# Optimization experiments

Hardware: AMD Instinct MI355X
Metric: run time of the kernel (lower is better)

The kernel has to match this reference:

```python
import jax, jax.numpy as jnp
import numpy as np

D_X, N_LAYERS, N_HEADS, D_OUT = 1024, 4, 16, 1024
D_H = D_X // N_HEADS
LN_EPS = 1e-5


def _layernorm(x, g, b):
    mu = jnp.mean(x, axis=-1, keepdims=True)
    var = jnp.var(x, axis=-1, keepdims=True)
    return (x - mu) * jax.lax.rsqrt(var + LN_EPS) * g + b


def setup_inputs() -> dict:
    key = jax.random.key(0)
    ks = jax.random.split(key, 12)
    s = 0.02
    inp = {
        "x": jax.random.normal(ks[0], (4, 1024, D_X), dtype=jnp.float32),
        # per-layer, per-head K/V projections (Q is unused by the original math)
        "Wk": jax.random.normal(ks[1], (N_LAYERS, N_HEADS, D_X, D_H), dtype=jnp.float32) * s,
        "bk": jnp.zeros((N_LAYERS, N_HEADS, D_H), dtype=jnp.float32),
        "Wv": jax.random.normal(ks[2], (N_LAYERS, N_HEADS, D_X, D_H), dtype=jnp.float32) * s,
        "bv": jnp.zeros((N_LAYERS, N_HEADS, D_H), dtype=jnp.float32),
        # per-layer FFN linear
        "Wl": jax.random.normal(ks[3], (N_LAYERS, D_X, D_X), dtype=jnp.float32) * s,
        "bl": jnp.zeros((N_LAYERS, D_X), dtype=jnp.float32),
        # per-layer LayerNorm params
        "g1": jnp.ones((N_LAYERS, D_X), dtype=jnp.float32),
        "b1": jnp.zeros((N_LAYERS, D_X), dtype=jnp.float32),
        "g2": jnp.ones((N_LAYERS, D_X), dtype=jnp.float32),
        "b2": jnp.zeros((N_LAYERS, D_X), dtype=jnp.float32),
        # output projection
        "Wo": jax.random.normal(ks[4], (D_X, D_OUT), dtype=jnp.float32) * s,
        "bo": jnp.zeros((D_OUT,), dtype=jnp.float32),
    }
    return inp


def reference(x, Wk, bk, Wv, bv, Wl, bl, g1, b1, g2, b2, Wo, bo):
    B, S, _ = x.shape
    scale = 1.0 / np.sqrt(D_H).astype(np.float32)
    for l in range(N_LAYERS):
        # batched across heads instead of the original per-head Python loop
        K = jnp.einsum("bsd,hdk->bhsk", x, Wk[l]) + bk[l][None, :, None, :]
        V = jnp.einsum("bsd,hdk->bhsk", x, Wv[l]) + bv[l][None, :, None, :]
        # faithful quirk: logits = K @ V^T (Q is never used in the source)
        logits = jnp.einsum("bhsk,bhtk->bhst", K, V) * scale
        attn = jnp.einsum("bhst,bhtk->bhsk", jax.nn.softmax(logits, axis=-1), V)
        attn = attn.transpose(0, 2, 1, 3).reshape(B, S, D_X)  # concat heads
        x = _layernorm(x + attn, g1[l], b1[l])
        ff = jax.nn.relu(jnp.einsum("bsd,de->bse", x, Wl[l]) + bl[l])
        x = _layernorm(x + ff, g2[l], b2[l])
    return jnp.einsum("bsd,do->bso", x, Wo) + bo
```

## Files before the change

### kernel.cpp

```cpp
#include <hip/hip_runtime.h>

typedef unsigned short u16;
typedef unsigned int u32;
typedef __attribute__((ext_vector_type(4))) float f32x4;
typedef __attribute__((ext_vector_type(8))) short short8;

#if __has_builtin(__builtin_amdgcn_exp2f)
#define EXP2(x) __builtin_amdgcn_exp2f(x)
#else
#define EXP2(x) exp2f(x)
#endif

#define SCALEK 0.18033688011112042f

__device__ __forceinline__ u16 f2b(float f) {
    unsigned u = __float_as_uint(f);
    u += 0x7fff + ((u >> 16) & 1);
    return (u16)(u >> 16);
}
__device__ __forceinline__ float b2f(u16 v) {
    return __uint_as_float(((unsigned)v) << 16);
}
__device__ __forceinline__ int swz(int byteoff) {
    return byteoff ^ (((byteoff >> 7) & 7) << 4);
}
__device__ __forceinline__ void gl16(const u16* g, u16* l) {
    __builtin_amdgcn_global_load_lds(
        (const __attribute__((address_space(1))) unsigned*)(g),
        (__attribute__((address_space(3))) unsigned*)(l), 16, 0, 0);
}
__device__ __forceinline__ u32 cvtpk(float lo, float hi) {
    u32 r;
    asm("v_cvt_pk_bf16_f32 %0, %1, %2" : "=v"(r) : "v"(lo), "v"(hi));
    return r;
}
__device__ __forceinline__ void plswap(u32& a, u32& b) {
    asm("v_permlane32_swap_b32 %0, %1" : "+v"(a), "+v"(b));
    asm("v_permlane16_swap_b32 %0, %1" : "+v"(a), "+v"(b));
}
#define MFMA16(a, b, c) __builtin_amdgcn_mfma_f32_16x16x32_bf16((a), (b), (c), 0, 0, 0)

__global__ __launch_bounds__(256) void pack_wkv_t(const float* __restrict__ W,
                                                  u16* __restrict__ out, int voff) {
    __shared__ float tile[32][33];
    int z = blockIdx.z; int l = z >> 4, h = z & 15;
    const float* ip = W + (size_t)z * 1024 * 64;
    u16* op = out + (size_t)l * 2048 * 1024 + (size_t)(voff + h * 64) * 1024;
    int tx = threadIdx.x & 31, ty = threadIdx.x >> 5;
    int d0 = blockIdx.y * 32, k0 = blockIdx.x * 32;
#pragma unroll
    for (int j = 0; j < 32; j += 8)
        tile[ty + j][tx] = ip[(size_t)(d0 + ty + j) * 64 + k0 + tx];
    __syncthreads();
#pragma unroll
    for (int j = 0; j < 32; j += 8)
        op[(size_t)(k0 + ty + j) * 1024 + d0 + tx] = f2b(tile[tx][ty + j]);
}

__global__ __launch_bounds__(256) void transpose_cvt(const float* __restrict__ in,
                                                     u16* __restrict__ out, int R, int C) {
    __shared__ float tile[32][33];
    const float* ip = in + (size_t)blockIdx.z * R * C;
    u16* op = out + (size_t)blockIdx.z * R * C;
    int tx = threadIdx.x & 31, ty = threadIdx.x >> 5;
    int r0 = blockIdx.y * 32, c0 = blockIdx.x * 32;
#pragma unroll
    for (int j = 0; j < 32; j += 8)
        tile[ty + j][tx] = ip[(size_t)(r0 + ty + j) * C + c0 + tx];
    __syncthreads();
#pragma unroll
    for (int j = 0; j < 32; j += 8)
        op[(size_t)(c0 + ty + j) * R + r0 + tx] = f2b(tile[tx][ty + j]);
}

__global__ __launch_bounds__(256) void cvt_bf16(const float* __restrict__ in,
                                                u16* __restrict__ out, int n) {
    int i = (blockIdx.x * 256 + threadIdx.x) * 4;
    if (i >= n) return;
    float4 v = *(const float4*)&in[i];
    ushort4 o = {f2b(v.x), f2b(v.y), f2b(v.z), f2b(v.w)};
    *(ushort4*)&out[i] = o;
}

template <int EPI, int BN>
__global__ __launch_bounds__(256) void gemm_bt(const u16* __restrict__ A,
                                               const u16* __restrict__ B,
                                               const float* __restrict__ bias1,
                                               const float* __restrict__ bias2, int split,
                                               void* __restrict__ Cv,
                                               u16* __restrict__ VTout,
                                               int M, int N, int K) {
    constexpr int NB = BN / 32;
    constexpr int BCH = BN * 4;
    __shared__ __align__(16) u16 lA[2][512 * 8];
    __shared__ __align__(16) u16 lB[2][BCH * 8];
    const int t = threadIdx.x;
    const int lane = t & 63, w = t >> 6;
    const int wr = w >> 1, wc = w & 1;
    const int g = lane >> 4, r = lane & 15;
    const int bid = blockIdx.x;
    const int rgn = bid & 7, idx = bid >> 3;
    const int by = (rgn >> 1) * 8 + (idx >> 3);
    const int bx = (rgn & 1) * 8 + (idx & 7);
    const int m0 = by * 128, n0 = bx * BN;

    const int c1 = w * 64 + lane;
    const int c2 = 256 + c1;
    const u16* Ap1 = A + (size_t)(m0 + (c1 & 127)) * K + (c1 >> 7) * 8;
    const u16* Ap2 = A + (size_t)(m0 + (c2 & 127)) * K + (c2 >> 7) * 8;
    const u16* Bp1 = B + (size_t)(n0 + (c1 & (BN - 1))) * K + (c1 / BN) * 8;
    const u16* Bp2 = B + (size_t)(n0 + (c2 & (BN - 1))) * K + (c2 / BN) * 8;

    f32x4 zero4 = {0.f, 0.f, 0.f, 0.f};
    f32x4 acc[4][NB];
#pragma unroll
    for (int m = 0; m < 4; ++m)
#pragma unroll
        for (int n = 0; n < NB; ++n) acc[m][n] = zero4;

#define GSTAGE(bufi, k0)                                        \
    do {                                                        \
        gl16(Ap1 + (k0), &lA[bufi][(w * 64) * 8]);              \
        gl16(Ap2 + (k0), &lA[bufi][(256 + w * 64) * 8]);        \
        gl16(Bp1 + (k0), &lB[bufi][(w * 64) * 8]);              \
        if constexpr (BN == 128)                                \
            gl16(Bp2 + (k0), &lB[bufi][(256 + w * 64) * 8]);    \
    } while (0)

    GSTAGE(0, 0);
    __syncthreads();
    const int nk = K >> 5;
    for (int kt = 0; kt < nk; ++kt) {
        const int cur = kt & 1;
        if (kt + 1 < nk) GSTAGE(cur ^ 1, (kt + 1) * 32);
        short8 af[4], bf[NB];
#pragma unroll
        for (int m = 0; m < 4; ++m)
            af[m] = *(const short8*)&lA[cur][(g * 128 + wr * 64 + m * 16 + r) * 8];
#pragma unroll
        for (int n = 0; n < NB; ++n)
            bf[n] = *(const short8*)&lB[cur][(g * BN + wc * (BN / 2) + n * 16 + r) * 8];
#pragma unroll
        for (int m = 0; m < 4; ++m)
#pragma unroll
            for (int n = 0; n < NB; ++n)
                acc[m][n] = MFMA16(af[m], bf[n], acc[m][n]);
        __syncthreads();
    }
#undef GSTAGE

#pragma unroll
    for (int m = 0; m < 4; ++m) {
        int row = m0 + wr * 64 + m * 16 + g * 4;
#pragma unroll
        for (int n = 0; n < NB; ++n) {
            int col = n0 + wc * (BN / 2) + n * 16 + r;
            float bv_ = (col < split) ? bias1[col] : bias2[col - split];
            if (EPI == 0) {
                float sc = (col < split) ? SCALEK : 1.0f;
                ushort4 qv;
                qv.x = f2b((acc[m][n][0] + bv_) * sc);
                qv.y = f2b((acc[m][n][1] + bv_) * sc);
                qv.z = f2b((acc[m][n][2] + bv_) * sc);
                qv.w = f2b((acc[m][n][3] + bv_) * sc);
                u16* Cb = (u16*)Cv;
                Cb[(size_t)(row + 0) * N + col] = qv.x;
                Cb[(size_t)(row + 1) * N + col] = qv.y;
                Cb[(size_t)(row + 2) * N + col] = qv.z;
                Cb[(size_t)(row + 3) * N + col] = qv.w;
                if (col >= split) {
                    int d = col - split, b_ = row >> 10, s = row & 1023;
                    *(ushort4*)&VTout[(((size_t)(b_ * 16) + (d >> 6)) * 64 + (d & 63)) * 1024 + s] = qv;
                }
            } else if (EPI == 1) {
                u16* Cb = (u16*)Cv;
#pragma unroll
                for (int i = 0; i < 4; ++i)
                    Cb[(size_t)(row + i) * N + col] = f2b(fmaxf(acc[m][n][i] + bv_, 0.f));
            } else {
#pragma unroll
                for (int i = 0; i < 4; ++i)
                    ((float*)Cv)[(size_t)(row + i) * N + col] = acc[m][n][i] + bv_;
            }
        }
    }
}

__global__ __launch_bounds__(512) void attn_kernel(const u16* __restrict__ KV,
                                                   const u16* __restrict__ VT,
                                                   u16* __restrict__ Out) {
    __shared__ __align__(16) u16 kt[2][512 * 8];
    __shared__ __align__(16) u16 vt[2][512 * 8];
    const int t = threadIdx.x;
    const int lane = t & 63, w = t >> 6;
    const int g = lane >> 4, r = lane & 15;
    const int d0 = blockIdx.x;
    const int q = d0 >> 3;
    const int bh = (d0 & 7) * 8 + (q >> 3), qb = q & 7;
    const int h = bh & 15, b = bh >> 4;
    const u16* Kbase = KV + (size_t)b * 1024 * 2048 + h * 64;
    const u16* Vbase = Kbase + 1024;
    const u16* VTbase = VT + ((size_t)(b * 16 + h)) * 64 * 1024;

    const int qrow = qb * 128 + w * 16 + r;
    const short8 qf0 = *(const short8*)&Kbase[(size_t)qrow * 2048 + g * 8];
    const short8 qf1 = *(const short8*)&Kbase[(size_t)qrow * 2048 + 32 + g * 8];

    const int row = t >> 3;
    const int colu = (((t & 7) * 16) ^ ((row & 7) << 4)) >> 1;
    const u16* Ksrc = Vbase + (size_t)row * 2048 + colu;
    const u16* Vsrc = VTbase + (size_t)row * 1024 + colu;

#define STAGE(bufi, t0)                                            \
    do {                                                           \
        gl16(Ksrc + (size_t)(t0) * 2048, &kt[bufi][(w * 64) * 8]); \
        gl16(Vsrc + (t0), &vt[bufi][(w * 64) * 8]);                \
    } while (0)

    STAGE(0, 0);

    float m = -1e30f, l = 0.f;
    f32x4 zero4 = {0.f, 0.f, 0.f, 0.f};
    f32x4 oacc[4];
#pragma unroll
    for (int n = 0; n < 4; ++n) oacc[n] = zero4;
    const int cbase = (lane & 48) | (g << 2);
    __syncthreads();

    for (int tt = 0; tt < 16; ++tt) {
        const int cur = tt & 1;
        if (tt < 15) STAGE(cur ^ 1, (tt + 1) * 64);
        const char* kbuf = (const char*)&kt[cur][0];
        const char* vbuf = (const char*)&vt[cur][0];

        f32x4 sfT[4];
#pragma unroll
        for (int n = 0; n < 4; ++n) sfT[n] = zero4;
#pragma unroll
        for (int ks = 0; ks < 2; ++ks) {
            const short8 qf = ks ? qf1 : qf0;
#pragma unroll
            for (int n = 0; n < 4; ++n) {
                short8 kf = *(const short8*)(kbuf + swz((n * 16 + r) * 128 + ks * 64 + g * 16));
                sfT[n] = MFMA16(kf, qf, sfT[n]);
            }
        }
        float rm = fmaxf(fmaxf(sfT[0][0], sfT[0][1]), fmaxf(sfT[0][2], sfT[0][3]));
        float r1 = fmaxf(fmaxf(sfT[1][0], sfT[1][1]), fmaxf(sfT[1][2], sfT[1][3]));
        float r2 = fmaxf(fmaxf(sfT[2][0], sfT[2][1]), fmaxf(sfT[2][2], sfT[2][3]));
        float r3 = fmaxf(fmaxf(sfT[3][0], sfT[3][1]), fmaxf(sfT[3][2], sfT[3][3]));
        rm = fmaxf(fmaxf(rm, r1), fmaxf(r2, r3));
        rm = fmaxf(rm, __shfl_xor(rm, 16, 64));
        rm = fmaxf(rm, __shfl_xor(rm, 32, 64));
        if (!__all(rm <= m + 8.f)) {
            float mn = fmaxf(m, rm);
            float cc = EXP2(m - mn);
            m = mn;
            l *= cc;
#pragma unroll
            for (int i = 0; i < 4; ++i) {
                float ci = __shfl(cc, cbase + i, 64);
#pragma unroll
                for (int n = 0; n < 4; ++n) oacc[n][i] *= ci;
            }
        }
        float rs = 0.f;
#pragma unroll
        for (int n = 0; n < 4; ++n)
#pragma unroll
            for (int i = 0; i < 4; ++i) {
                float p = EXP2(sfT[n][i] - m);
                sfT[n][i] = p;
                rs += p;
            }
        rs += __shfl_xor(rs, 16, 64);
        rs += __shfl_xor(rs, 32, 64);
        l += rs;
        u32 wpk[4][2];
#pragma unroll
        for (int n = 0; n < 4; ++n) {
            wpk[n][0] = cvtpk(sfT[n][0], sfT[n][1]);
            wpk[n][1] = cvtpk(sfT[n][2], sfT[n][3]);
        }
#pragma unroll
        for (int ks = 0; ks < 2; ++ks) {
            u32 a0 = wpk[2 * ks][0], a2 = wpk[2 * ks + 1][0];
            plswap(a0, a2);
            u32 a1 = wpk[2 * ks][1], a3 = wpk[2 * ks + 1][1];
            plswap(a1, a3);
            uint4 av;
            av.x = a0; av.y = a1; av.z = a2; av.w = a3;
            union { uint4 u; short8 s; } uc;
            uc.u = av;
            const short8 af = uc.s;
#pragma unroll
            for (int n = 0; n < 4; ++n) {
                short8 vf = *(const short8*)(vbuf + swz((n * 16 + r) * 128 + ks * 64 + g * 16));
                oacc[n] = MFMA16(af, vf, oacc[n]);
            }
        }
        __syncthreads();
    }
#undef STAGE

#pragma unroll
    for (int i = 0; i < 4; ++i) {
        float li = 1.f / __shfl(l, cbase + i, 64);
        int orow = b * 1024 + qb * 128 + w * 16 + g * 4 + i;
#pragma unroll
        for (int n = 0; n < 4; ++n)
            Out[(size_t)orow * 1024 + h * 64 + n * 16 + r] = f2b(oacc[n][i] * li);
    }
}

__global__ __launch_bounds__(256) void ln_kernel(const u16* __restrict__ xin,
                                                 const u16* __restrict__ addin,
                                                 const float* __restrict__ gamma,
                                                 const float* __restrict__ beta,
                                                 u16* __restrict__ xbout) {
    const int row = blockIdx.x, t = threadIdx.x;
    const size_t base = (size_t)row * 1024;
    ushort4 xu = *(const ushort4*)&xin[base + t * 4];
    ushort4 au = *(const ushort4*)&addin[base + t * 4];
    float v0 = b2f(xu.x) + b2f(au.x), v1 = b2f(xu.y) + b2f(au.y);
    float v2 = b2f(xu.z) + b2f(au.z), v3 = b2f(xu.w) + b2f(au.w);
    float s = v0 + v1 + v2 + v3;
    __shared__ float red[4];
    const int lane = t & 63, w = t >> 6;
#pragma unroll
    for (int off = 32; off; off >>= 1) s += __shfl_xor(s, off, 64);
    if (lane == 0) red[w] = s;
    __syncthreads();
    float mean = (red[0] + red[1] + red[2] + red[3]) * (1.f / 1024.f);
    __syncthreads();
    float d0 = v0 - mean, d1 = v1 - mean, d2 = v2 - mean, d3 = v3 - mean;
    float sq = d0 * d0 + d1 * d1 + d2 * d2 + d3 * d3;
#pragma unroll
    for (int off = 32; off; off >>= 1) sq += __shfl_xor(sq, off, 64);
    if (lane == 0) red[w] = sq;
    __syncthreads();
    float var = (red[0] + red[1] + red[2] + red[3]) * (1.f / 1024.f);
    float rstd = rsqrtf(var + 1e-5f);
    float4 gv = *(const float4*)&gamma[t * 4];
    float4 bv = *(const float4*)&beta[t * 4];
    ushort4 o;
    o.x = f2b(d0 * rstd * gv.x + bv.x);
    o.y = f2b(d1 * rstd * gv.y + bv.y);
    o.z = f2b(d2 * rstd * gv.z + bv.z);
    o.w = f2b(d3 * rstd * gv.w + bv.w);
    *(ushort4*)&xbout[base + t * 4] = o;
}

extern "C" void kernel_launch(void* const* d_in, const int* in_sizes, int n_in,
                              void* d_out, int out_size, void* d_ws, size_t ws_size,
                              hipStream_t stream) {
    const float* x  = (const float*)d_in[0];
    const float* Wk = (const float*)d_in[1];
    const float* bk = (const float*)d_in[2];
    const float* Wv = (const float*)d_in[3];
    const float* bv = (const float*)d_in[4];
    const float* Wl = (const float*)d_in[5];
    const float* bl = (const float*)d_in[6];
    const float* g1 = (const float*)d_in[7];
    const float* b1 = (const float*)d_in[8];
    const float* g2 = (const float*)d_in[9];
    const float* b2 = (const float*)d_in[10];
    const float* Wo = (const float*)d_in[11];
    const float* bo = (const float*)d_in[12];

    char* ws = (char*)d_ws;
    u16* Wkvb = (u16*)ws;  ws += (size_t)4 * 2048 * 1024 * 2;
    u16* Wlb  = (u16*)ws;  ws += (size_t)4 * 1024 * 1024 * 2;
    u16* Wob  = (u16*)ws;  ws += (size_t)1024 * 1024 * 2;
    u16* xb   = (u16*)ws;  ws += (size_t)4096 * 1024 * 2;
    u16* KVb  = (u16*)ws;  ws += (size_t)4096 * 2048 * 2;
    u16* VTb  = (u16*)ws;  ws += (size_t)4096 * 1024 * 2;
    u16* tmpb = (u16*)ws;  ws += (size_t)4096 * 1024 * 2;

    pack_wkv_t<<<dim3(2, 32, 64), 256, 0, stream>>>(Wk, Wkvb, 0);
    pack_wkv_t<<<dim3(2, 32, 64), 256, 0, stream>>>(Wv, Wkvb, 1024);
    transpose_cvt<<<dim3(32, 32, 4), 256, 0, stream>>>(Wl, Wlb, 1024, 1024);
    transpose_cvt<<<dim3(32, 32, 1), 256, 0, stream>>>(Wo, Wob, 1024, 1024);
    cvt_bf16<<<dim3(4096), 256, 0, stream>>>(x, xb, 4096 * 1024);

    for (int l = 0; l < 4; ++l) {
        gemm_bt<0, 128><<<dim3(512), 256, 0, stream>>>(
            xb, Wkvb + (size_t)l * 2048 * 1024, bk + l * 1024, bv + l * 1024, 1024,
            (void*)KVb, VTb, 4096, 2048, 1024);
        attn_kernel<<<dim3(512), 512, 0, stream>>>(KVb, VTb, tmpb);
        ln_kernel<<<dim3(4096), 256, 0, stream>>>(
            xb, tmpb, g1 + l * 1024, b1 + l * 1024, xb);
        gemm_bt<1, 64><<<dim3(512), 256, 0, stream>>>(
            xb, Wlb + (size_t)l * 1024 * 1024, bl + l * 1024, bl + l * 1024, 1024,
            (void*)tmpb, nullptr, 4096, 1024, 1024);
        ln_kernel<<<dim3(4096), 256, 0, stream>>>(
            xb, tmpb, g2 + l * 1024, b2 + l * 1024, xb);
    }
    gemm_bt<2, 64><<<dim3(512), 256, 0, stream>>>(
        xb, Wob, bo, bo, 1024, d_out, nullptr, 4096, 1024, 1024);
}
```

Before: 503.6 us.

## Give each wave private LDS buffers in GEMM, removing block barriers

The GEMM kernel now has every wave load its own A and B slices into a private LDS region. That removes the need for __syncthreads in the K loop, and manual vmcnt/lgkmcnt waits replace the barrier. Prefetch depth moves to two stages issued after the fragment reads, so global loads can overlap the MFMAs without any cross-wave synchronization. The cost is that the wc=0/1 wave pairs load the same A data twice and the wr pairs load the same B data twice. This doubles global/L2 traffic and raises LDS footprint, which may reduce occupancy.

Result: slower. 818.8 us (+62.6%).

```diff
diff --git a/kernel.cpp b/kernel.cpp
--- a/kernel.cpp
+++ b/kernel.cpp
@@ -83,17 +83,20 @@
 }
 
 template <int EPI, int BN>
-__global__ __launch_bounds__(256) void gemm_bt(const u16* __restrict__ A,
+__global__ __launch_bounds__(256) void gemm_wp(const u16* __restrict__ A,
                                                const u16* __restrict__ B,
                                                const float* __restrict__ bias1,
                                                const float* __restrict__ bias2, int split,
                                                void* __restrict__ Cv,
                                                u16* __restrict__ VTout,
                                                int M, int N, int K) {
-    constexpr int NB = BN / 32;
-    constexpr int BCH = BN * 4;
-    __shared__ __align__(16) u16 lA[2][512 * 8];
-    __shared__ __align__(16) u16 lB[2][BCH * 8];
+    constexpr int WBN = BN / 2;
+    constexpr int NB = WBN / 16;
+    constexpr int NLD = 4 + NB;
+    constexpr int ABU = 2048;
+    constexpr int BBU = WBN * 32;
+    constexpr int WSTR = 2 * (ABU + BBU);
+    __shared__ __align__(16) u16 sh[4 * WSTR];
     const int t = threadIdx.x;
     const int lane = t & 63, w = t >> 6;
     const int wr = w >> 1, wc = w & 1;
@@ -104,12 +107,33 @@
     const int bx = (rgn & 1) * 8 + (idx & 7);
     const int m0 = by * 128, n0 = bx * BN;
 
-    const int c1 = w * 64 + lane;
-    const int c2 = 256 + c1;
-    const u16* Ap1 = A + (size_t)(m0 + (c1 & 127)) * K + (c1 >> 7) * 8;
-    const u16* Ap2 = A + (size_t)(m0 + (c2 & 127)) * K + (c2 >> 7) * 8;
-    const u16* Bp1 = B + (size_t)(n0 + (c1 & (BN - 1))) * K + (c1 / BN) * 8;
-    const u16* Bp2 = B + (size_t)(n0 + (c2 & (BN - 1))) * K + (c2 / BN) * 8;
+    u16* wb = sh + w * WSTR;
+    u16* bA[2] = {wb, wb + ABU + BBU};
+    u16* bB[2] = {wb + ABU, wb + ABU + BBU + ABU};
+
+    const u16* sAp = A + (size_t)(m0 + wr * 64 + lane) * K;
+    const u16* sBp;
+    if constexpr (BN == 128)
+        sBp = B + (size_t)(n0 + wc * 64 + lane) * K;
+    else
+        sBp = B + (size_t)(n0 + wc * 32 + (lane & 31)) * K + (lane >> 5) * 8;
+
+#define WSTAGE(bi, k0)                                              \
+    do {                                                            \
+        gl16(sAp + (k0) + 0 * 8, bA[bi] + 0 * 512);                 \
+        gl16(sAp + (k0) + 1 * 8, bA[bi] + 1 * 512);                 \
+        gl16(sAp + (k0) + 2 * 8, bA[bi] + 2 * 512);                 \
+        gl16(sAp + (k0) + 3 * 8, bA[bi] + 3 * 512);                 \
+        if constexpr (BN == 128) {                                  \
+            gl16(sBp + (k0) + 0 * 8, bB[bi] + 0 * 512);             \
+            gl16(sBp + (k0) + 1 * 8, bB[bi] + 1 * 512);             \
+            gl16(sBp + (k0) + 2 * 8, bB[bi] + 2 * 512);             \
+            gl16(sBp + (k0) + 3 * 8, bB[bi] + 3 * 512);             \
+        } else {                                                    \
+            gl16(sBp + (k0) + 0 * 16, bB[bi] + 0 * 512);            \
+            gl16(sBp + (k0) + 1 * 16, bB[bi] + 1 * 512);            \
+        }                                                           \
+    } while (0)
 
     f32x4 zero4 = {0.f, 0.f, 0.f, 0.f};
     f32x4 acc[4][NB];
@@ -118,43 +142,41 @@
 #pragma unroll
         for (int n = 0; n < NB; ++n) acc[m][n] = zero4;
 
-#define GSTAGE(bufi, k0)                                        \
-    do {                                                        \
-        gl16(Ap1 + (k0), &lA[bufi][(w * 64) * 8]);              \
-        gl16(Ap2 + (k0), &lA[bufi][(256 + w * 64) * 8]);        \
-        gl16(Bp1 + (k0), &lB[bufi][(w * 64) * 8]);              \
-        if constexpr (BN == 128)                                \
-            gl16(Bp2 + (k0), &lB[bufi][(256 + w * 64) * 8]);    \
-    } while (0)
-
-    GSTAGE(0, 0);
-    __syncthreads();
+    WSTAGE(0, 0);
+    WSTAGE(1, 32);
     const int nk = K >> 5;
     for (int kt = 0; kt < nk; ++kt) {
         const int cur = kt & 1;
-        if (kt + 1 < nk) GSTAGE(cur ^ 1, (kt + 1) * 32);
+        if (kt + 1 < nk) {
+            asm volatile("s_waitcnt vmcnt(%0)" :: "i"(NLD) : "memory");
+        } else {
+            asm volatile("s_waitcnt vmcnt(0)" ::: "memory");
+        }
+        __builtin_amdgcn_sched_barrier(0);
         short8 af[4], bf[NB];
 #pragma unroll
         for (int m = 0; m < 4; ++m)
-            af[m] = *(const short8*)&lA[cur][(g * 128 + wr * 64 + m * 16 + r) * 8];
+            af[m] = *(const short8*)&bA[cur][(g * 64 + m * 16 + r) * 8];
 #pragma unroll
         for (int n = 0; n < NB; ++n)
-            bf[n] = *(const short8*)&lB[cur][(g * BN + wc * (BN / 2) + n * 16 + r) * 8];
+            bf[n] = *(const short8*)&bB[cur][(g * WBN + n * 16 + r) * 8];
+        asm volatile("s_waitcnt lgkmcnt(0)" ::: "memory");
+        __builtin_amdgcn_sched_barrier(0);
+        if (kt + 2 < nk) WSTAGE(cur, (kt + 2) * 32);
 #pragma unroll
         for (int m = 0; m < 4; ++m)
 #pragma unroll
             for (int n = 0; n < NB; ++n)
                 acc[m][n] = MFMA16(af[m], bf[n], acc[m][n]);
-        __syncthreads();
     }
-#undef GSTAGE
+#undef WSTAGE
 
 #pragma unroll
     for (int m = 0; m < 4; ++m) {
         int row = m0 + wr * 64 + m * 16 + g * 4;
 #pragma unroll
         for (int n = 0; n < NB; ++n) {
-            int col = n0 + wc * (BN / 2) + n * 16 + r;
+            int col = n0 + wc * WBN + n * 16 + r;
             float bv_ = (col < split) ? bias1[col] : bias2[col - split];
             if (EPI == 0) {
                 float sc = (col < split) ? SCALEK : 1.0f;
@@ -384,18 +406,18 @@
     cvt_bf16<<<dim3(4096), 256, 0, stream>>>(x, xb, 4096 * 1024);
 
     for (int l = 0; l < 4; ++l) {
-        gemm_bt<0, 128><<<dim3(512), 256, 0, stream>>>(
+        gemm_wp<0, 128><<<dim3(512), 256, 0, stream>>>(
             xb, Wkvb + (size_t)l * 2048 * 1024, bk + l * 1024, bv + l * 1024, 1024,
             (void*)KVb, VTb, 4096, 2048, 1024);
         attn_kernel<<<dim3(512), 512, 0, stream>>>(KVb, VTb, tmpb);
         ln_kernel<<<dim3(4096), 256, 0, stream>>>(
             xb, tmpb, g1 + l * 1024, b1 + l * 1024, xb);
-        gemm_bt<1, 64><<<dim3(512), 256, 0, stream>>>(
+        gemm_wp<1, 64><<<dim3(512), 256, 0, stream>>>(
             xb, Wlb + (size_t)l * 1024 * 1024, bl + l * 1024, bl + l * 1024, 1024,
             (void*)tmpb, nullptr, 4096, 1024, 1024);
         ln_kernel<<<dim3(4096), 256, 0, stream>>>(
             xb, tmpb, g2 + l * 1024, b2 + l * 1024, xb);
     }
-    gemm_bt<2, 64><<<dim3(512), 256, 0, stream>>>(
+    gemm_wp<2, 64><<<dim3(512), 256, 0, stream>>>(
         xb, Wob, bo, bo, 1024, d_out, nullptr, 4096, 1024, 1024);
 }
```
